# Kernel optimization log

Hardware: AMD Instinct MI355X
Metric: run time of the kernel (lower is better)

## Reference

```python
import jax, jax.numpy as jnp
import numpy as np

B, T, I, H = 32, 1024, 1024, 1024


def _init_cell(key, in_size, hidden):
    k = 1.0 / np.sqrt(hidden)
    k1, k2, k3, k4 = jax.random.split(key, 4)
    Wih = jax.random.uniform(k1, (4 * hidden, in_size), jnp.float32, -k, k)
    Whh = jax.random.uniform(k2, (4 * hidden, hidden), jnp.float32, -k, k)
    bih = jax.random.uniform(k3, (4 * hidden,), jnp.float32, -k, k)
    bhh = jax.random.uniform(k4, (4 * hidden,), jnp.float32, -k, k)
    return Wih, Whh, bih, bhh


def setup_inputs() -> dict:
    key = jax.random.key(0)
    kx, kf, kr = jax.random.split(key, 3)
    x = jax.random.normal(kx, (B, T, I), jnp.float32)
    h0 = jnp.zeros((B, H), jnp.float32)
    c0 = jnp.zeros((B, H), jnp.float32)
    Wih_f, Whh_f, bih_f, bhh_f = _init_cell(kf, I, H)
    Wih_r, Whh_r, bih_r, bhh_r = _init_cell(kr, I, H)
    return {"x": x, "h0": h0, "c0": c0,
            "Wih_f": Wih_f, "Whh_f": Whh_f, "bih_f": bih_f, "bhh_f": bhh_f,
            "Wih_r": Wih_r, "Whh_r": Whh_r, "bih_r": bih_r, "bhh_r": bhh_r}


def _lstm_scan(xs, h0, c0, Wih, Whh, bih, bhh, reverse):
    # xs: [T, B, I]; PyTorch LSTMCell gate order: i, f, g, o
    def step(carry, xt):
        h, c = carry
        gates = xt @ Wih.T + bih + h @ Whh.T + bhh  # [B, 4H]
        i, f, g, o = jnp.split(gates, 4, axis=-1)
        c_new = jax.nn.sigmoid(f) * c + jax.nn.sigmoid(i) * jnp.tanh(g)
        h_new = jax.nn.sigmoid(o) * jnp.tanh(c_new)
        return (h_new, c_new), None

    (hT, cT), _ = jax.lax.scan(step, (h0, c0), xs, reverse=reverse)
    return hT, cT


def reference(x, h0, c0, Wih_f, Whh_f, bih_f, bhh_f, Wih_r, Whh_r, bih_r, bhh_r):
    xs = jnp.swapaxes(x, 0, 1)  # [T, B, I]
    hf, _ = _lstm_scan(xs, h0, c0, Wih_f, Whh_f, bih_f, bhh_f, reverse=False)
    # reversed(x.unbind(1)) == processing time steps from T-1 down to 0
    hr, _ = _lstm_scan(xs, h0, c0, Wih_r, Whh_r, bih_r, bhh_r, reverse=True)
    return (hf, hr)
```

## Files before the change

kernel.cpp:

```cpp
#include <hip/hip_runtime.h>
#include <hip/hip_bf16.h>
#include <cstdint>
#include <cstddef>

typedef unsigned short u16;
typedef unsigned long long u64;
typedef __attribute__((ext_vector_type(8))) _Float16 h8;
typedef __attribute__((ext_vector_type(4))) float f32x4;
typedef __attribute__((ext_vector_type(4))) unsigned u32x4;

#define NB 32
#define NT 1024
#define NH 1024
#define TCH 128
#define NCH 8

#define O_XB   0ull
#define O_WIH  67108864ull
#define O_WHHP 83886080ull
#define O_BIAS 117440512ull
#define O_HBUF 117473280ull
#define O_CST  117735424ull
#define O_FLG  117997568ull
#define O_GX   118030336ull
#define DSTRIDE_CH   16777216ull
#define DSTRIDE_HALF 33554432ull
#define DSTRIDE_FULL 134217728ull
#define WS_NEED_HALF (O_GX + 2ull * DSTRIDE_HALF * 2ull)
#define WS_NEED_FULL (O_GX + 2ull * DSTRIDE_FULL * 2ull)

__device__ __forceinline__ u16 f2h(float f){
  union { _Float16 h; u16 u; } v; v.h = (_Float16)f; return v.u;
}
__device__ __forceinline__ float h2f(u16 b){
  union { u16 u; _Float16 h; } v; v.u = b; return (float)v.h;
}
__device__ __forceinline__ float sig_f(float x){ return 1.0f / (1.0f + __expf(-x)); }
__device__ __forceinline__ float tanh_f(float x){ return 1.0f - 2.0f / (1.0f + __expf(2.0f * x)); }

__device__ __forceinline__ void g2l16(const void* g, void* l){
  __builtin_amdgcn_global_load_lds(
      (const __attribute__((address_space(1))) unsigned int*)g,
      (__attribute__((address_space(3))) unsigned int*)l, 16, 0, 0);
}
__device__ __forceinline__ void g2l16c(const void* g, void* l){
  __builtin_amdgcn_global_load_lds(
      (const __attribute__((address_space(1))) unsigned int*)g,
      (__attribute__((address_space(3))) unsigned int*)l, 16, 0, 17);
}
__device__ __forceinline__ void store16_llc(void* p, u32x4 v){
  asm volatile("global_store_dwordx4 %0, %1, off sc0 sc1"
               :: "v"((unsigned long long)(uintptr_t)p), "v"(v) : "memory");
}

__device__ __forceinline__ float sel4(float s0, float s1, float s2, float s3, int k){
  float a = (k & 1) ? s1 : s0;
  float b = (k & 1) ? s3 : s2;
  return (k & 2) ? b : a;
}

__device__ __forceinline__ int img_off(int lr, int bo){
  return lr * 2048 + (bo ^ ((((lr & 7) ^ ((bo >> 8) & 7))) << 4));
}

__global__ void k_cvt(const float* __restrict__ src, u16* __restrict__ dst, int n){
  int i = (blockIdx.x * blockDim.x + threadIdx.x) * 4;
  int stride = gridDim.x * blockDim.x * 4;
  for (; i < n; i += stride){
    float4 v = *(const float4*)(src + i);
    uint2 p;
    p.x = (unsigned)f2h(v.x) | ((unsigned)f2h(v.y) << 16);
    p.y = (unsigned)f2h(v.z) | ((unsigned)f2h(v.w) << 16);
    *(uint2*)(dst + i) = p;
  }
}

__global__ void k_pack_whh(const float* __restrict__ whh_f, const float* __restrict__ whh_r,
                           u16* __restrict__ dst){
  int bx = blockIdx.x;
  int dir = bx >> 8, rem = bx & 255;
  int jg = rem >> 1, ni = rem & 1;
  const float* whh = dir ? whh_r : whh_f;
  int tid = threadIdx.x;
  int lane = tid & 63, wq = tid >> 6;
  int c = lane & 15;
  int n = (c >> 2) * 1024 + jg * 8 + ni * 4 + (c & 3);
  int kkb = (lane >> 4) * 8;
  size_t fb = (((size_t)dir * 128 + jg) * 2 + ni) * 32;
  for (int q = 0; q < 8; q++){
    int ks = wq * 8 + q;
    const float4* p = (const float4*)(whh + (size_t)n * 1024 + ks * 32 + kkb);
    float4 w0 = p[0], w1 = p[1];
    float w[8] = {w0.x, w0.y, w0.z, w0.w, w1.x, w1.y, w1.z, w1.w};
    unsigned hh[4];
    #pragma unroll
    for (int e = 0; e < 4; e++)
      hh[e] = (unsigned)f2h(w[2*e]) | ((unsigned)f2h(w[2*e+1]) << 16);
    uint4* dh = (uint4*)(dst + (fb + (size_t)ks) * 512 + lane * 8);
    *dh = make_uint4(hh[0], hh[1], hh[2], hh[3]);
  }
}

__global__ void k_init(const float* __restrict__ h0, const float* __restrict__ c0,
                       const float* __restrict__ bih_f, const float* __restrict__ bhh_f,
                       const float* __restrict__ bih_r, const float* __restrict__ bhh_r,
                       char* __restrict__ hbuf, float* __restrict__ cst,
                       float* __restrict__ bias, int* __restrict__ flg){
  int i = blockIdx.x * blockDim.x + threadIdx.x;
  int stride = gridDim.x * blockDim.x;
  for (int k = i; k < 32768; k += stride){
    int b = k >> 10, j = k & 1023;
    int lr = b & 15, mhb = b >> 4;
    u16 v = f2h(h0[k]);
    int off = img_off(lr, 2 * j);
    *(u16*)(hbuf + (size_t)((0 * 2 + mhb) * 2) * 32768 + off) = v;
    *(u16*)(hbuf + (size_t)((1 * 2 + mhb) * 2) * 32768 + off) = v;
    float cv = c0[k];
    cst[k] = cv;
    cst[32768 + k] = cv;
  }
  for (int k = i; k < 8192; k += stride){
    if (k < 4096) bias[k] = bih_f[k] + bhh_f[k];
    else          bias[k] = bih_r[k - 4096] + bhh_r[k - 4096];
  }
  for (int k = i; k < 8192; k += stride) flg[k] = 0;
}

__global__ __launch_bounds__(256, 2) void k_gemm(const u16* __restrict__ xb,
                                                 const u16* __restrict__ wih,
                                                 const float* __restrict__ bias,
                                                 u16* __restrict__ gx, int chunk,
                                                 int tOff, size_t dirStride){
  __shared__ u16 smem[2 * 16384];
  const int tid = threadIdx.x;
  const int lane = tid & 63, wid = tid >> 6;
  const int mi = wid >> 1, ni = wid & 1;
  const int c = lane & 15, rg = lane >> 4;
  const int n0 = blockIdx.x * 128;
  const int m0 = blockIdx.y * 128;
  const int dir = blockIdx.z;
  const u16* wd = wih + (size_t)dir * 4194304;

  f32x4 acc[4][4] = {};

  auto stage = [&](int buf, int k0){
    #pragma unroll
    for (int q = 0; q < 8; q++){
      int f = wid * 8 + q;
      int ks = f & 1;
      int kk = k0 + ks * 32 + rg * 8;
      const u16* src;
      if (f < 16){
        int rowloc = (f >> 1) * 16 + c;
        int tl = (m0 + rowloc) >> 5;
        int bb = rowloc & 31;
        int tg = dir ? (1023 - chunk * TCH - tl) : (chunk * TCH + tl);
        src = xb + (size_t)(bb * 1024 + tg) * 1024 + kk;
      } else {
        int nt = (f - 16) >> 1;
        src = wd + (size_t)(n0 + nt * 16 + c) * 1024 + kk;
      }
      g2l16((const void*)src, (void*)(smem + buf * 16384 + f * 512));
    }
  };

  stage(0, 0);
  asm volatile("s_waitcnt vmcnt(0)" ::: "memory");
  __syncthreads();

  for (int it = 0; it < 16; it++){
    int cur = it & 1;
    if (it < 15) stage(cur ^ 1, (it + 1) * 64);
    const u16* bp = smem + cur * 16384;
    #pragma unroll
    for (int ks = 0; ks < 2; ks++){
      h8 a[4], b[4];
      #pragma unroll
      for (int im = 0; im < 4; im++)
        a[im] = *(const h8*)(bp + ((mi * 4 + im) * 2 + ks) * 512 + lane * 8);
      #pragma unroll
      for (int in_ = 0; in_ < 4; in_++)
        b[in_] = *(const h8*)(bp + 8192 + ((ni * 4 + in_) * 2 + ks) * 512 + lane * 8);
      #pragma unroll
      for (int im = 0; im < 4; im++)
        #pragma unroll
        for (int in_ = 0; in_ < 4; in_++)
          acc[im][in_] = __builtin_amdgcn_mfma_f32_16x16x32_f16(a[im], b[in_], acc[im][in_], 0, 0, 0);
    }
    asm volatile("s_waitcnt vmcnt(0)" ::: "memory");
    __syncthreads();
  }

  u16* T = (u16*)smem;
  const float* bd = bias + dir * 4096;
  #pragma unroll
  for (int in_ = 0; in_ < 4; in_++){
    int nnLocal = (ni * 4 + in_) * 16 + c;
    float bv = bd[n0 + nnLocal];
    #pragma unroll
    for (int im = 0; im < 4; im++){
      #pragma unroll
      for (int r = 0; r < 4; r++){
        int row = (mi * 4 + im) * 16 + rg * 4 + r;
        T[row * 128 + nnLocal] = f2h(acc[im][in_][r] + bv);
      }
    }
  }
  __syncthreads();
  u16* gxd = gx + (size_t)dir * dirStride;
  const int nprBase = ((n0 & 1023) >> 3) * 32 + ((n0 >> 10) << 3);
  #pragma unroll
  for (int q = 0; q < 8; q++){
    int flat = q * 256 + tid;
    int row = flat >> 4, c16 = flat & 15;
    u32x4 v = *(const u32x4*)(T + row * 128 + c16 * 8);
    *(u32x4*)(gxd + (size_t)(tOff * 32 + m0 + row) * 4096 + nprBase + c16 * 32) = v;
  }
}

__global__ __launch_bounds__(256, 1) void k_rnn(const u16* __restrict__ gx,
                                                const u16* __restrict__ whhp,
                                                char* __restrict__ hbuf,
                                                float* __restrict__ cstate,
                                                float* __restrict__ dout,
                                                int* __restrict__ flg,
                                                int s0, int bar0, int nsteps,
                                                size_t dirStride){
  __shared__ char smem[32768];
  __shared__ __align__(16) u16 tb[16][16];
  __shared__ int lflag[2];
  const int tid = threadIdx.x;
  const int lane = tid & 63, wid = tid >> 6;
  const int bx = blockIdx.x;
  const int dir = bx >> 7, mh = (bx >> 6) & 1, ug = bx & 63;
  const int grp = dir * 2 + mh;
  const int c = lane & 15, rg = lane >> 4;
  const int g = c >> 2, jj = c & 3;
  const int u = ug * 16 + wid * 4 + jj;
  const int jg = ug * 2 + (wid >> 1), ni = wid & 1;

  h8 Bh[32];
  {
    size_t fb = (((size_t)dir * 128 + jg) * 2 + ni) * 32;
    #pragma unroll
    for (int ks = 0; ks < 32; ks++)
      Bh[ks] = *(const h8*)(whhp + (fb + ks) * 512 + lane * 8);
  }

  float cst[4];
  #pragma unroll
  for (int r = 0; r < 4; r++)
    cst[r] = cstate[(size_t)dir * 32768 + (size_t)(mh * 16 + rg * 4 + r) * 1024 + u];

  const int npr = (u >> 3) * 32 + g * 8 + (u & 7);
  int* flags = flg + grp * 2048;

  if (tid == 0){ lflag[0] = 0; lflag[1] = 0; }
  __syncthreads();

  u16 gxu[4];
  {
    const size_t gof = (size_t)dir * dirStride + npr;
    #pragma unroll
    for (int r = 0; r < 4; r++)
      gxu[r] = gx[gof + (size_t)(mh * 16 + rg * 4 + r) * 4096];
  }

  for (int t = 0; t < nsteps; t++){
    const int s = s0 + t;
    const char* img_r = hbuf + (size_t)(grp * 2 + (s & 1)) * 32768;
    char* img_w = hbuf + (size_t)(grp * 2 + ((s + 1) & 1)) * 32768;
    const unsigned tgt = (unsigned)(bar0 + t);

    if (wid == 0){
      if (t > 0){
        int* fp = flags + (lane & 31) * 32;
        while (true){
          int v = __hip_atomic_load(fp, __ATOMIC_RELAXED, __HIP_MEMORY_SCOPE_AGENT);
          if (__all((unsigned)v >= tgt)) break;
        }
        asm volatile("" ::: "memory");
      }
      #pragma unroll
      for (int i = 0; i < 16; i++)
        g2l16c(img_r + i * 2048 + lane * 16, smem + i * 2048 + lane * 16);
      asm volatile("s_waitcnt vmcnt(0)" ::: "memory");
      __hip_atomic_store(&lflag[0], t + 1, __ATOMIC_RELEASE, __HIP_MEMORY_SCOPE_WORKGROUP);
    } else if (wid == 1){
      if (t > 0){
        int* fp = flags + (32 + (lane & 31)) * 32;
        while (true){
          int v = __hip_atomic_load(fp, __ATOMIC_RELAXED, __HIP_MEMORY_SCOPE_AGENT);
          if (__all((unsigned)v >= tgt)) break;
        }
        asm volatile("" ::: "memory");
      }
      #pragma unroll
      for (int i = 0; i < 16; i++)
        g2l16c(img_r + i * 2048 + 1024 + lane * 16, smem + i * 2048 + 1024 + lane * 16);
      asm volatile("s_waitcnt vmcnt(0)" ::: "memory");
      __hip_atomic_store(&lflag[1], t + 1, __ATOMIC_RELEASE, __HIP_MEMORY_SCOPE_WORKGROUP);
    }

    u16 gxn[4];
    if (t < nsteps - 1){
      const size_t gof = (size_t)dir * dirStride + (size_t)(t + 1) * 131072 + npr;
      #pragma unroll
      for (int r = 0; r < 4; r++)
        gxn[r] = gx[gof + (size_t)(mh * 16 + rg * 4 + r) * 4096];
    }

    f32x4 ae = {0.f,0.f,0.f,0.f}, ao = {0.f,0.f,0.f,0.f};
    const int abase = c * 2048;
    while (__hip_atomic_load(&lflag[0], __ATOMIC_ACQUIRE, __HIP_MEMORY_SCOPE_WORKGROUP) < t + 1) {}
    __builtin_amdgcn_sched_barrier(0);
    #pragma unroll
    for (int kp = 0; kp < 8; kp++){
      int b0 = (kp * 2) * 64 + rg * 16;
      int b1 = (kp * 2 + 1) * 64 + rg * 16;
      int ad0 = abase + (b0 ^ ((((c & 7) ^ ((b0 >> 8) & 7))) << 4));
      int ad1 = abase + (b1 ^ ((((c & 7) ^ ((b1 >> 8) & 7))) << 4));
      h8 x0 = *(const h8*)(smem + ad0);
      h8 x1 = *(const h8*)(smem + ad1);
      ae = __builtin_amdgcn_mfma_f32_16x16x32_f16(x0, Bh[kp * 2], ae, 0, 0, 0);
      ao = __builtin_amdgcn_mfma_f32_16x16x32_f16(x1, Bh[kp * 2 + 1], ao, 0, 0, 0);
    }
    while (__hip_atomic_load(&lflag[1], __ATOMIC_ACQUIRE, __HIP_MEMORY_SCOPE_WORKGROUP) < t + 1) {}
    __builtin_amdgcn_sched_barrier(0);
    #pragma unroll
    for (int kp = 8; kp < 16; kp++){
      int b0 = (kp * 2) * 64 + rg * 16;
      int b1 = (kp * 2 + 1) * 64 + rg * 16;
      int ad0 = abase + (b0 ^ ((((c & 7) ^ ((b0 >> 8) & 7))) << 4));
      int ad1 = abase + (b1 ^ ((((c & 7) ^ ((b1 >> 8) & 7))) << 4));
      h8 x0 = *(const h8*)(smem + ad0);
      h8 x1 = *(const h8*)(smem + ad1);
      ae = __builtin_amdgcn_mfma_f32_16x16x32_f16(x0, Bh[kp * 2], ae, 0, 0, 0);
      ao = __builtin_amdgcn_mfma_f32_16x16x32_f16(x1, Bh[kp * 2 + 1], ao, 0, 0, 0);
    }

    #pragma unroll
    for (int r = 0; r < 4; r++){
      float v = (ae[r] + ao[r]) + h2f(gxu[r]);
      float act = (g == 2) ? tanh_f(v) : sig_f(v);
      float a4  = __int_as_float(__builtin_amdgcn_ds_swizzle(__float_as_int(act), 0x101F));
      float a8  = __int_as_float(__builtin_amdgcn_ds_swizzle(__float_as_int(act), 0x201F));
      float a12 = __int_as_float(__builtin_amdgcn_ds_swizzle(__float_as_int(act), 0x301F));
      float i_s = sel4(act, a4, a8, a12, g);
      float f_s = sel4(act, a4, a8, a12, g ^ 1);
      float g_t = sel4(act, a4, a8, a12, g ^ 2);
      float o_s = sel4(act, a4, a8, a12, g ^ 3);
      float cn = f_s * cst[r] + i_s * g_t;
      cst[r] = cn;
      float hn = o_s * tanh_f(cn);
      if (g == 0){
        int lr = rg * 4 + r;
        tb[lr][wid * 4 + jj] = f2h(hn);
        if (s == 1023)
          dout[(size_t)dir * 32768 + (size_t)(mh * 16 + lr) * 1024 + u] = hn;
        if (t == nsteps - 1)
          cstate[(size_t)dir * 32768 + (size_t)(mh * 16 + lr) * 1024 + u] = cn;
      }
    }
    __syncthreads();

    if (wid == 3){
      if (lane < 32){
        int lr = lane >> 1, half = lane & 1;
        u32x4 v = *(const u32x4*)&tb[lr][half * 8];
        store16_llc(img_w + img_off(lr, ug * 32 + half * 16), v);
      }
      asm volatile("s_waitcnt vmcnt(0)" ::: "memory");
      if (lane == 0 && t < nsteps - 1)
        __hip_atomic_store(&flags[ug * 32], bar0 + t + 1,
                           __ATOMIC_RELAXED, __HIP_MEMORY_SCOPE_AGENT);
    }

    if (t < nsteps - 1){
      #pragma unroll
      for (int r = 0; r < 4; r++) gxu[r] = gxn[r];
    }
  }
}

extern "C" void kernel_launch(void* const* d_in, const int* in_sizes, int n_in,
                              void* d_out, int out_size, void* d_ws, size_t ws_size,
                              hipStream_t stream){
  const float* x     = (const float*)d_in[0];
  const float* h0    = (const float*)d_in[1];
  const float* c0    = (const float*)d_in[2];
  const float* Wih_f = (const float*)d_in[3];
  const float* Whh_f = (const float*)d_in[4];
  const float* bih_f = (const float*)d_in[5];
  const float* bhh_f = (const float*)d_in[6];
  const float* Wih_r = (const float*)d_in[7];
  const float* Whh_r = (const float*)d_in[8];
  const float* bih_r = (const float*)d_in[9];
  const float* bhh_r = (const float*)d_in[10];
  float* out = (float*)d_out;

  char* ws = (char*)d_ws;
  u16*   xb    = (u16*)(ws + O_XB);
  u16*   wih   = (u16*)(ws + O_WIH);
  u16*   whhp  = (u16*)(ws + O_WHHP);
  float* bias  = (float*)(ws + O_BIAS);
  char*  hbuf  = (char*)(ws + O_HBUF);
  float* cstw  = (float*)(ws + O_CST);
  int*   flg   = (int*)(ws + O_FLG);
  u16*   gx    = (u16*)(ws + O_GX);

  k_cvt<<<2048, 256, 0, stream>>>(x, xb, 32 * 1024 * 1024);
  k_cvt<<<512, 256, 0, stream>>>(Wih_f, wih, 4096 * 1024);
  k_cvt<<<512, 256, 0, stream>>>(Wih_r, wih + 4194304, 4096 * 1024);
  k_pack_whh<<<512, 256, 0, stream>>>(Whh_f, Whh_r, whhp);
  k_init<<<64, 256, 0, stream>>>(h0, c0, bih_f, bhh_f, bih_r, bhh_r, hbuf, cstw, bias, flg);

  if (ws_size >= WS_NEED_FULL){
    for (int g = 0; g < NCH; g++)
      k_gemm<<<dim3(32, 32, 2), 256, 0, stream>>>(xb, wih, bias, gx, g,
                                                  g * TCH, (size_t)DSTRIDE_FULL);
    k_rnn<<<dim3(256), dim3(256), 0, stream>>>(gx, whhp, hbuf, cstw, out, flg,
                                               0, 0, NT, (size_t)DSTRIDE_FULL);
  } else if (ws_size >= WS_NEED_HALF){
    for (int c2 = 0; c2 < 4; c2++){
      k_gemm<<<dim3(32, 32, 2), 256, 0, stream>>>(xb, wih, bias, gx, 2 * c2,
                                                  0, (size_t)DSTRIDE_HALF);
      k_gemm<<<dim3(32, 32, 2), 256, 0, stream>>>(xb, wih, bias, gx, 2 * c2 + 1,
                                                  128, (size_t)DSTRIDE_HALF);
      k_rnn<<<dim3(256), dim3(256), 0, stream>>>(gx, whhp, hbuf, cstw, out, flg,
                                                 c2 * 256, c2 * 255, 256,
                                                 (size_t)DSTRIDE_HALF);
    }
  } else {
    for (int ch = 0; ch < NCH; ch++){
      k_gemm<<<dim3(32, 32, 2), 256, 0, stream>>>(xb, wih, bias, gx, ch,
                                                  0, (size_t)DSTRIDE_CH);
      k_rnn<<<dim3(256), dim3(256), 0, stream>>>(gx, whhp, hbuf, cstw, out, flg,
                                                 ch * TCH, ch * (TCH - 1), TCH,
                                                 (size_t)DSTRIDE_CH);
    }
  }
}
```

Before: 4.981 ms.

## Overlap input-projection GEMM with recurrent steps via fused double-buffered kernel

Replaces the full-precompute path with a double-buffered scheme: a single fused launch runs the 256 persistent recurrent blocks on one gate buffer while extra blocks compute the next 256-step input-projection GEMM into the other buffer. This hides GEMM time behind the latency-bound recurrence and halves workspace needs. The risk is that the GEMM blocks compete with the recurrent blocks for CUs and memory bandwidth, and the recurrent blocks rely on being co-resident for their flag-based sync. The fused kernel also uses 65 KB of shared memory with launch_bounds 2, which could change occupancy.

Result: faster. 4.704 ms (median of 2 runs) (-5.6%).

```diff
diff --git a/kernel.cpp b/kernel.cpp
--- a/kernel.cpp
+++ b/kernel.cpp
@@ -25,9 +25,9 @@
 #define O_GX   118030336ull
 #define DSTRIDE_CH   16777216ull
 #define DSTRIDE_HALF 33554432ull
-#define DSTRIDE_FULL 134217728ull
-#define WS_NEED_HALF (O_GX + 2ull * DSTRIDE_HALF * 2ull)
-#define WS_NEED_FULL (O_GX + 2ull * DSTRIDE_FULL * 2ull)
+#define GXBUF_ELEMS  (2ull * DSTRIDE_HALF)
+#define WS_NEED_HALF (O_GX + GXBUF_ELEMS * 2ull)
+#define WS_NEED_DBUF (O_GX + 2ull * GXBUF_ELEMS * 2ull)
 
 __device__ __forceinline__ u16 f2h(float f){
   union { _Float16 h; u16 u; } v; v.h = (_Float16)f; return v.u;
@@ -126,19 +126,19 @@
   for (int k = i; k < 8192; k += stride) flg[k] = 0;
 }
 
-__global__ __launch_bounds__(256, 2) void k_gemm(const u16* __restrict__ xb,
-                                                 const u16* __restrict__ wih,
-                                                 const float* __restrict__ bias,
-                                                 u16* __restrict__ gx, int chunk,
-                                                 int tOff, size_t dirStride){
-  __shared__ u16 smem[2 * 16384];
+__device__ __forceinline__ void gemm_body(u16* smem,
+                                          const u16* __restrict__ xb,
+                                          const u16* __restrict__ wih,
+                                          const float* __restrict__ bias,
+                                          u16* __restrict__ gx, int chunk,
+                                          int tOff, size_t dirStride,
+                                          int bxp, int byp, int dir){
   const int tid = threadIdx.x;
   const int lane = tid & 63, wid = tid >> 6;
   const int mi = wid >> 1, ni = wid & 1;
   const int c = lane & 15, rg = lane >> 4;
-  const int n0 = blockIdx.x * 128;
-  const int m0 = blockIdx.y * 128;
-  const int dir = blockIdx.z;
+  const int n0 = bxp * 128;
+  const int m0 = byp * 128;
   const u16* wd = wih + (size_t)dir * 4194304;
 
   f32x4 acc[4][4] = {};
@@ -191,7 +191,7 @@
     __syncthreads();
   }
 
-  u16* T = (u16*)smem;
+  u16* T = smem;
   const float* bd = bias + dir * 4096;
   #pragma unroll
   for (int in_ = 0; in_ < 4; in_++){
@@ -218,21 +218,28 @@
   }
 }
 
-__global__ __launch_bounds__(256, 1) void k_rnn(const u16* __restrict__ gx,
-                                                const u16* __restrict__ whhp,
-                                                char* __restrict__ hbuf,
-                                                float* __restrict__ cstate,
-                                                float* __restrict__ dout,
-                                                int* __restrict__ flg,
-                                                int s0, int bar0, int nsteps,
-                                                size_t dirStride){
-  __shared__ char smem[32768];
-  __shared__ __align__(16) u16 tb[16][16];
-  __shared__ int lflag[2];
+__global__ __launch_bounds__(256, 2) void k_gemm(const u16* __restrict__ xb,
+                                                 const u16* __restrict__ wih,
+                                                 const float* __restrict__ bias,
+                                                 u16* __restrict__ gx, int chunk,
+                                                 int tOff, size_t dirStride){
+  __shared__ u16 smem[2 * 16384];
+  gemm_body(smem, xb, wih, bias, gx, chunk, tOff, dirStride,
+            blockIdx.x, blockIdx.y, blockIdx.z);
+}
+
+__device__ __forceinline__ void rnn_body(char* smem, u16 (*tb)[16], int* lflag,
+                                         const u16* __restrict__ gx,
+                                         const u16* __restrict__ whhp,
+                                         char* __restrict__ hbuf,
+                                         float* __restrict__ cstate,
+                                         float* __restrict__ dout,
+                                         int* __restrict__ flg,
+                                         int s0, int bar0, int nsteps,
+                                         size_t dirStride, int rb){
   const int tid = threadIdx.x;
   const int lane = tid & 63, wid = tid >> 6;
-  const int bx = blockIdx.x;
-  const int dir = bx >> 7, mh = (bx >> 6) & 1, ug = bx & 63;
+  const int dir = rb >> 7, mh = (rb >> 6) & 1, ug = rb & 63;
   const int grp = dir * 2 + mh;
   const int c = lane & 15, rg = lane >> 4;
   const int g = c >> 2, jj = c & 3;
@@ -383,6 +390,53 @@
   }
 }
 
+__global__ __launch_bounds__(256, 1) void k_rnn(const u16* __restrict__ gx,
+                                                const u16* __restrict__ whhp,
+                                                char* __restrict__ hbuf,
+                                                float* __restrict__ cstate,
+                                                float* __restrict__ dout,
+                                                int* __restrict__ flg,
+                                                int s0, int bar0, int nsteps,
+                                                size_t dirStride){
+  __shared__ char smem[32768];
+  __shared__ __align__(16) u16 tb[16][16];
+  __shared__ int lflag[2];
+  rnn_body(smem, tb, lflag, gx, whhp, hbuf, cstate, dout, flg,
+           s0, bar0, nsteps, dirStride, blockIdx.x);
+}
+
+__global__ __launch_bounds__(256, 2) void k_fused(const u16* __restrict__ xb,
+                                                  const u16* __restrict__ wih,
+                                                  const float* __restrict__ bias,
+                                                  const u16* __restrict__ whhp,
+                                                  char* __restrict__ hbuf,
+                                                  float* __restrict__ cstate,
+                                                  float* __restrict__ dout,
+                                                  int* __restrict__ flg,
+                                                  const u16* __restrict__ gxR,
+                                                  u16* __restrict__ gxW,
+                                                  int c256){
+  __shared__ __align__(16) char S[65536 + 1024];
+  const int bid = blockIdx.x;
+  if (bid < 256){
+    char* smem = S;
+    u16 (*tb)[16] = (u16(*)[16])(S + 65536);
+    int* lflag = (int*)(S + 65536 + 512);
+    rnn_body(smem, tb, lflag, gxR, whhp, hbuf, cstate, dout, flg,
+             c256 * 256, c256 * 255, 256, (size_t)DSTRIDE_HALF, bid);
+  } else {
+    int gid = bid - 256;
+    int sub = gid >> 11;
+    int rem = gid & 2047;
+    int dir = rem >> 10;
+    int r2  = rem & 1023;
+    int byp = r2 >> 5, bxp = r2 & 31;
+    gemm_body((u16*)S, xb, wih, bias, gxW,
+              (c256 + 1) * 2 + sub, sub * 128, (size_t)DSTRIDE_HALF,
+              bxp, byp, dir);
+  }
+}
+
 extern "C" void kernel_launch(void* const* d_in, const int* in_sizes, int n_in,
                               void* d_out, int out_size, void* d_ws, size_t ws_size,
                               hipStream_t stream){
@@ -407,7 +461,8 @@
   char*  hbuf  = (char*)(ws + O_HBUF);
   float* cstw  = (float*)(ws + O_CST);
   int*   flg   = (int*)(ws + O_FLG);
-  u16*   gx    = (u16*)(ws + O_GX);
+  u16*   gxA   = (u16*)(ws + O_GX);
+  u16*   gxB   = gxA + GXBUF_ELEMS;
 
   k_cvt<<<2048, 256, 0, stream>>>(x, xb, 32 * 1024 * 1024);
   k_cvt<<<512, 256, 0, stream>>>(Wih_f, wih, 4096 * 1024);
@@ -415,27 +470,31 @@
   k_pack_whh<<<512, 256, 0, stream>>>(Whh_f, Whh_r, whhp);
   k_init<<<64, 256, 0, stream>>>(h0, c0, bih_f, bhh_f, bih_r, bhh_r, hbuf, cstw, bias, flg);
 
-  if (ws_size >= WS_NEED_FULL){
-    for (int g = 0; g < NCH; g++)
-      k_gemm<<<dim3(32, 32, 2), 256, 0, stream>>>(xb, wih, bias, gx, g,
-                                                  g * TCH, (size_t)DSTRIDE_FULL);
-    k_rnn<<<dim3(256), dim3(256), 0, stream>>>(gx, whhp, hbuf, cstw, out, flg,
-                                               0, 0, NT, (size_t)DSTRIDE_FULL);
+  if (ws_size >= WS_NEED_DBUF){
+    k_gemm<<<dim3(32, 32, 2), 256, 0, stream>>>(xb, wih, bias, gxA, 0, 0, (size_t)DSTRIDE_HALF);
+    k_gemm<<<dim3(32, 32, 2), 256, 0, stream>>>(xb, wih, bias, gxA, 1, 128, (size_t)DSTRIDE_HALF);
+    for (int c = 0; c < 4; c++){
+      const u16* gxR = (c & 1) ? gxB : gxA;
+      u16*       gxW = (c & 1) ? gxA : gxB;
+      int grid = 256 + (c < 3 ? 4096 : 0);
+      k_fused<<<dim3(grid), dim3(256), 0, stream>>>(xb, wih, bias, whhp, hbuf, cstw,
+                                                    out, flg, gxR, gxW, c);
+    }
   } else if (ws_size >= WS_NEED_HALF){
     for (int c2 = 0; c2 < 4; c2++){
-      k_gemm<<<dim3(32, 32, 2), 256, 0, stream>>>(xb, wih, bias, gx, 2 * c2,
+      k_gemm<<<dim3(32, 32, 2), 256, 0, stream>>>(xb, wih, bias, gxA, 2 * c2,
                                                   0, (size_t)DSTRIDE_HALF);
-      k_gemm<<<dim3(32, 32, 2), 256, 0, stream>>>(xb, wih, bias, gx, 2 * c2 + 1,
+      k_gemm<<<dim3(32, 32, 2), 256, 0, stream>>>(xb, wih, bias, gxA, 2 * c2 + 1,
                                                   128, (size_t)DSTRIDE_HALF);
-      k_rnn<<<dim3(256), dim3(256), 0, stream>>>(gx, whhp, hbuf, cstw, out, flg,
+      k_rnn<<<dim3(256), dim3(256), 0, stream>>>(gxA, whhp, hbuf, cstw, out, flg,
                                                  c2 * 256, c2 * 255, 256,
                                                  (size_t)DSTRIDE_HALF);
     }
   } else {
     for (int ch = 0; ch < NCH; ch++){
-      k_gemm<<<dim3(32, 32, 2), 256, 0, stream>>>(xb, wih, bias, gx, ch,
+      k_gemm<<<dim3(32, 32, 2), 256, 0, stream>>>(xb, wih, bias, gxA, ch,
                                                   0, (size_t)DSTRIDE_CH);
-      k_rnn<<<dim3(256), dim3(256), 0, stream>>>(gx, whhp, hbuf, cstw, out, flg,
+      k_rnn<<<dim3(256), dim3(256), 0, stream>>>(gxA, whhp, hbuf, cstw, out, flg,
                                                  ch * TCH, ch * (TCH - 1), TCH,
                                                  (size_t)DSTRIDE_CH);
     }
```
